# Performance work log

Hardware: AMD Instinct MI355X
Metric: run time of the kernel (lower is better)

## Reference

```python
import jax, jax.numpy as jnp
import numpy as np

EPS = 1e-5  # torch BatchNorm1d default


def _bn(v, gamma, beta):
    # BatchNorm1d in training mode, applied independently per timestep:
    # normalize over the batch axis (axis=1) with biased variance.
    mean = jnp.mean(v, axis=1, keepdims=True)
    var = jnp.var(v, axis=1, keepdims=True)
    return (v - mean) * jax.lax.rsqrt(var + EPS) * gamma + beta


def _ligru_layer(x, h0, Wxz, bxz, gz, bz, Whz, bhz, Wxh, bxh, gh, bh, Whh, bhh):
    # x: [T,B,I]. Precompute the input-side linear+batchnorm for all timesteps
    # (BN is per-timestep over batch, so it has no time dependence).
    nxz = _bn(jnp.einsum('tbi,hi->tbh', x, Wxz) + bxz, gz, bz)  # [T,B,H]
    nxh = _bn(jnp.einsum('tbi,hi->tbh', x, Wxh) + bxh, gh, bh)  # [T,B,H]

    def step(h, inp):
        xz_t, xh_t = inp
        z = jax.nn.sigmoid(xz_t + h @ Whz.T + bhz)
        cand = jax.nn.relu(xh_t + h @ Whh.T + bhh)
        h_new = z * h + (1.0 - z) * cand
        return h_new, h_new

    h_last, hs = jax.lax.scan(step, h0, (nxz, nxh))
    return hs, h_last  # [T,B,H], [B,H]


def setup_inputs() -> dict:
    key = jax.random.key(0)
    T, B, I, H, L = 512, 32, 1024, 1024, 2
    ks = jax.random.split(key, 6)
    s = 1.0 / np.sqrt(H)
    return {
        'x': jax.random.normal(ks[0], (T, B, I), jnp.float32),
        'h0': jnp.zeros((B, H), jnp.float32),
        'Wxz': jax.random.normal(ks[1], (L, H, I), jnp.float32) * s,
        'bxz': jnp.zeros((L, H), jnp.float32),
        'gz': jnp.ones((L, H), jnp.float32),
        'bz': jnp.zeros((L, H), jnp.float32),
        'Whz': jax.random.normal(ks[2], (L, H, H), jnp.float32) * s,
        'bhz': jnp.zeros((L, H), jnp.float32),
        'Wxh': jax.random.normal(ks[3], (L, H, I), jnp.float32) * s,
        'bxh': jnp.zeros((L, H), jnp.float32),
        'gh': jnp.ones((L, H), jnp.float32),
        'bh': jnp.zeros((L, H), jnp.float32),
        'Whh': jax.random.normal(ks[4], (L, H, H), jnp.float32) * s,
        'bhh': jnp.zeros((L, H), jnp.float32),
    }


def reference(x, h0, Wxz, bxz, gz, bz, Whz, bhz, Wxh, bxh, gh, bh, Whh, bhh):
    L = Wxz.shape[0]
    h_hist = []
    for l in range(L):  # small fixed layer loop (structurally distinct params)
        x, h_last = _ligru_layer(x, h0,
                                 Wxz[l], bxz[l], gz[l], bz[l], Whz[l], bhz[l],
                                 Wxh[l], bxh[l], gh[l], bh[l], Whh[l], bhh[l])
        h_hist.append(h_last)
    return x, jnp.stack(h_hist, axis=0)  # ([T,B,H], [L,B,H])
```

## Files before the change

kernel.cpp:

```cpp
#include <hip/hip_runtime.h>


typedef unsigned short u16;
typedef unsigned int   u32;
typedef unsigned long long u64;
typedef __attribute__((ext_vector_type(8))) short bf16x8;
typedef __attribute__((ext_vector_type(4))) float f32x4;
typedef __attribute__((ext_vector_type(2))) float f32x2;
typedef __attribute__((ext_vector_type(4))) unsigned int u32x4;

#define TSTEPS 512
#define BATCH  32
#define HDIM   1024
#define MROWS  (TSTEPS * BATCH)
#define KP     2048
#define NWG    64

__device__ __forceinline__ u16 f2bf(float f) {
  u32 u = __float_as_uint(f);
  return (u16)((u + 0x7FFFu + ((u >> 16) & 1u)) >> 16);
}
__device__ __forceinline__ float bf2f(u16 h) {
  return __uint_as_float(((u32)h) << 16);
}

__global__ void cast_split(const float* __restrict__ src, u16* __restrict__ dst, int total) {
  int idx = blockIdx.x * 256 + threadIdx.x;
  if (idx >= total) return;
  int m = idx >> 10, k = idx & 1023;
  float v = src[idx];
  u16 hi = f2bf(v);
  u16 lo = f2bf(v - bf2f(hi));
  dst[(size_t)m * KP + k] = hi;
  dst[(size_t)m * KP + 1024 + k] = lo;
}

__device__ __forceinline__ void stage16(const u16* g, u16* l) {
  __builtin_amdgcn_global_load_lds((const __attribute__((address_space(1))) u32*)g,
                                   (__attribute__((address_space(3))) u32*)l, 16, 0, 0);
}

__global__ __launch_bounds__(256) void gemm_bt(
    const u16* __restrict__ A,
    const u16* __restrict__ Wa, const u16* __restrict__ Wb,
    float* __restrict__ Ca, float* __restrict__ Cb) {
  constexpr int BK = 64;
  const u16* W = blockIdx.z ? Wb : Wa;
  float*     C = blockIdx.z ? Cb : Ca;
  const int m0 = blockIdx.y * 128;
  const int n0 = blockIdx.x * 128;
  __shared__ __align__(16) u16 As[128 * BK];
  __shared__ __align__(16) u16 Bs[128 * BK];
  const int tid  = threadIdx.x;
  const int lane = tid & 63;
  const int wv   = tid >> 6;
  const int wm   = wv >> 1, wn = wv & 1;
  const int srow = tid >> 3;
  const int scol = (tid & 7) * 8;
  const int frow = lane & 15;
  const int kcol = (lane >> 4) * 8;

  f32x4 z4 = {0.f, 0.f, 0.f, 0.f};
  f32x4 acc[4][4];
#pragma unroll
  for (int i = 0; i < 4; ++i)
#pragma unroll
    for (int j = 0; j < 4; ++j) acc[i][j] = z4;

  for (int k0 = 0; k0 < KP; k0 += BK) {
#pragma unroll
    for (int i = 0; i < 4; ++i)
      stage16(A + (size_t)(m0 + i * 32 + srow) * KP + k0 + scol, &As[(i * 32 + srow) * BK + scol]);
#pragma unroll
    for (int i = 0; i < 4; ++i)
      stage16(W + (size_t)(n0 + i * 32 + srow) * KP + k0 + scol, &Bs[(i * 32 + srow) * BK + scol]);
    __syncthreads();
#pragma unroll
    for (int kk = 0; kk < 2; ++kk) {
      bf16x8 av[4], bv[4];
#pragma unroll
      for (int i = 0; i < 4; ++i)
        av[i] = *(const bf16x8*)&As[(wm * 64 + i * 16 + frow) * BK + kk * 32 + kcol];
#pragma unroll
      for (int j = 0; j < 4; ++j)
        bv[j] = *(const bf16x8*)&Bs[(wn * 64 + j * 16 + frow) * BK + kk * 32 + kcol];
#pragma unroll
      for (int i = 0; i < 4; ++i)
#pragma unroll
        for (int j = 0; j < 4; ++j)
          acc[i][j] = __builtin_amdgcn_mfma_f32_16x16x32_bf16(av[i], bv[j], acc[i][j], 0, 0, 0);
    }
    __syncthreads();
  }
#pragma unroll
  for (int i = 0; i < 4; ++i)
#pragma unroll
    for (int j = 0; j < 4; ++j) {
      int n  = n0 + wn * 64 + j * 16 + (lane & 15);
      int mb = m0 + wm * 64 + i * 16 + (lane >> 4) * 4;
#pragma unroll
      for (int r = 0; r < 4; ++r)
        C[(size_t)(mb + r) * HDIM + n] = acc[i][j][r];
    }
}

__global__ void bn_inplace(float* __restrict__ Pz, float* __restrict__ Ph,
                           const float* __restrict__ gz, const float* __restrict__ bz, const float* __restrict__ bhz,
                           const float* __restrict__ gh, const float* __restrict__ bh, const float* __restrict__ bhh) {
  float*       P    = blockIdx.y ? Ph  : Pz;
  const float* gam  = blockIdx.y ? gh  : gz;
  const float* bet  = blockIdx.y ? bh  : bz;
  const float* brec = blockIdx.y ? bhh : bhz;
  int idx = blockIdx.x * 256 + threadIdx.x;
  int h = idx & 1023;
  size_t base = (size_t)(idx >> 10) * (BATCH * HDIM) + h;
  float v[BATCH];
  float s = 0.f;
#pragma unroll
  for (int b = 0; b < BATCH; ++b) { v[b] = P[base + (size_t)b * HDIM]; s += v[b]; }
  float mean = s * (1.f / BATCH);
  float q = 0.f;
#pragma unroll
  for (int b = 0; b < BATCH; ++b) { float d = v[b] - mean; q += d * d; }
  float inv = rsqrtf(q * (1.f / BATCH) + 1e-5f) * gam[h];
  float add = bet[h] + brec[h];
#pragma unroll
  for (int b = 0; b < BATCH; ++b)
    P[base + (size_t)b * HDIM] = (v[b] - mean) * inv + add;
}

__global__ void init_bar(u32* flags) { flags[threadIdx.x] = 0; }

__global__ __launch_bounds__(256, 1) void ligru_rec(
    const float* __restrict__ nxz, const float* __restrict__ nxh,
    const float* __restrict__ Whz, const float* __restrict__ Whh,
    const float* __restrict__ h0,
    u16*   __restrict__ hs_bf,
    float* __restrict__ hs_f,
    float* __restrict__ hlast,
    u32*   __restrict__ hbufw,
    u32*   __restrict__ flags) {
  const int g    = blockIdx.x;
  const int c0   = g * 16;
  const int tid  = threadIdx.x;
  const int lane = tid & 63;
  const int wv   = tid >> 6;
  const int half = wv >> 1;
  const int ksec = wv & 1;
  const int r    = lane & 15;
  const int ko   = lane >> 4;

  __shared__ float part[2][2][2][16][17];

  bf16x8 wz_hi[16], wz_lo[16], wh_hi[16], wh_lo[16];
  {
    const float* zrow = Whz + (size_t)(c0 + r) * HDIM;
    const float* hrow = Whh + (size_t)(c0 + r) * HDIM;
#pragma unroll
    for (int kk = 0; kk < 16; ++kk) {
      int kb = ksec * 512 + ko * 8 + kk * 32;
      f32x4 z0 = *(const f32x4*)(zrow + kb);
      f32x4 z1 = *(const f32x4*)(zrow + kb + 4);
      f32x4 h0v = *(const f32x4*)(hrow + kb);
      f32x4 h1v = *(const f32x4*)(hrow + kb + 4);
      bf16x8 zh, zl, hh, hl;
#pragma unroll
      for (int j = 0; j < 4; ++j) {
        u16 a = f2bf(z0[j]);  zh[j]   = (short)a;  zl[j]   = (short)f2bf(z0[j] - bf2f(a));
        u16 b = f2bf(z1[j]);  zh[4+j] = (short)b;  zl[4+j] = (short)f2bf(z1[j] - bf2f(b));
        u16 c = f2bf(h0v[j]); hh[j]   = (short)c;  hl[j]   = (short)f2bf(h0v[j] - bf2f(c));
        u16 d = f2bf(h1v[j]); hh[4+j] = (short)d;  hl[4+j] = (short)f2bf(h1v[j] - bf2f(d));
      }
      wz_hi[kk] = zh; wz_lo[kk] = zl; wh_hi[kk] = hh; wh_lo[kk] = hl;
    }
  }

  const int bb = tid >> 3;
  const int cp = tid & 7;
  const int bh_ = bb >> 4, br_ = bb & 15;
  float hr0 = h0[(size_t)bb * HDIM + c0 + 2 * cp];
  float hr1 = h0[(size_t)bb * HDIM + c0 + 2 * cp + 1];
  {
    u32 p = (u32)f2bf(hr0) | ((u32)f2bf(hr1) << 16);
    __hip_atomic_store(hbufw + (size_t)bb * 512 + g * 8 + cp, p,
                       __ATOMIC_RELAXED, __HIP_MEMORY_SCOPE_AGENT);
  }
  __syncthreads();
  if (tid == 0)
    __hip_atomic_store(&flags[g], 1u, __ATOMIC_RELAXED, __HIP_MEMORY_SCOPE_AGENT);
  {
    for (;;) {
      u32 f = __hip_atomic_load(&flags[lane], __ATOMIC_RELAXED, __HIP_MEMORY_SCOPE_AGENT);
      if (__all(f >= 1u)) break;
    }
  }

  const size_t hb64base = (size_t)(half * 16 + r) * 256 + ksec * 128 + ko * 2;
  f32x4 z4 = {0.f, 0.f, 0.f, 0.f};

  f32x2 nxz_c = *(const f32x2*)(nxz + (size_t)bb * HDIM + c0 + 2 * cp);
  f32x2 nxh_c = *(const f32x2*)(nxh + (size_t)bb * HDIM + c0 + 2 * cp);

  for (int t = 0; t < TSTEPS; ++t) {
    const u64* hb64 = (const u64*)(hbufw + (size_t)(t & 1) * (BATCH * 512));
    u32*       hbn  = hbufw + (size_t)((t + 1) & 1) * (BATCH * 512);

    asm volatile("" ::: "memory");
    const u64* hbp = hb64 + hb64base;
    u32x4 hw4[16];
#pragma unroll
    for (int kk = 0; kk < 16; ++kk)
      asm volatile("global_load_dwordx4 %0, %1, off offset:%2 sc0 sc1"
                   : "=v"(hw4[kk])
                   : "v"(hbp), "i"(kk * 64));
    asm volatile("s_waitcnt vmcnt(0)" ::: "memory");
    __builtin_amdgcn_sched_barrier(0);

    int tn = (t + 1 < TSTEPS) ? t + 1 : t;
    f32x2 nxz_n = *(const f32x2*)(nxz + (size_t)(tn * BATCH + bb) * HDIM + c0 + 2 * cp);
    f32x2 nxh_n = *(const f32x2*)(nxh + (size_t)(tn * BATCH + bb) * HDIM + c0 + 2 * cp);

    f32x4 az0 = z4, az1 = z4, ac0 = z4, ac1 = z4;
#pragma unroll
    for (int kk = 0; kk < 16; ++kk) {
      union { u32x4 q; bf16x8 v; } a;
      a.q = hw4[kk];
      az0 = __builtin_amdgcn_mfma_f32_16x16x32_bf16(a.v, wz_hi[kk], az0, 0, 0, 0);
      az1 = __builtin_amdgcn_mfma_f32_16x16x32_bf16(a.v, wz_lo[kk], az1, 0, 0, 0);
      ac0 = __builtin_amdgcn_mfma_f32_16x16x32_bf16(a.v, wh_hi[kk], ac0, 0, 0, 0);
      ac1 = __builtin_amdgcn_mfma_f32_16x16x32_bf16(a.v, wh_lo[kk], ac1, 0, 0, 0);
    }
    f32x4 sz = az0 + az1;
    f32x4 sc = ac0 + ac1;

#pragma unroll
    for (int reg = 0; reg < 4; ++reg) {
      part[0][ksec][half][ko * 4 + reg][r] = sz[reg];
      part[1][ksec][half][ko * 4 + reg][r] = sc[reg];
    }
    __syncthreads();

    float zp0 = part[0][0][bh_][br_][2 * cp]     + part[0][1][bh_][br_][2 * cp]     + nxz_c[0];
    float zp1 = part[0][0][bh_][br_][2 * cp + 1] + part[0][1][bh_][br_][2 * cp + 1] + nxz_c[1];
    float cp0 = part[1][0][bh_][br_][2 * cp]     + part[1][1][bh_][br_][2 * cp]     + nxh_c[0];
    float cp1 = part[1][0][bh_][br_][2 * cp + 1] + part[1][1][bh_][br_][2 * cp + 1] + nxh_c[1];
    float zg0 = 1.f / (1.f + __expf(-zp0));
    float zg1 = 1.f / (1.f + __expf(-zp1));
    float cd0 = fmaxf(cp0, 0.f);
    float cd1 = fmaxf(cp1, 0.f);
    float hn0 = zg0 * hr0 + (1.f - zg0) * cd0;
    float hn1 = zg1 * hr1 + (1.f - zg1) * cd1;
    hr0 = hn0; hr1 = hn1;

    u16 hi0 = f2bf(hn0), hi1 = f2bf(hn1);
    u32 p = (u32)hi0 | ((u32)hi1 << 16);
    __hip_atomic_store(hbn + (size_t)bb * 512 + g * 8 + cp, p,
                       __ATOMIC_RELAXED, __HIP_MEMORY_SCOPE_AGENT);
    __syncthreads();
    if (tid == 0)
      __hip_atomic_store(&flags[g], (u32)(t + 2), __ATOMIC_RELAXED, __HIP_MEMORY_SCOPE_AGENT);

    if (hs_f) {
      f32x2 o = {hn0, hn1};
      *(f32x2*)(hs_f + (size_t)(t * BATCH + bb) * HDIM + c0 + 2 * cp) = o;
    } else {
      size_t row = (size_t)(t * BATCH + bb) * KP;
      *(u32*)(hs_bf + row + c0 + 2 * cp) = p;
      u32 plo = (u32)f2bf(hn0 - bf2f(hi0)) | ((u32)f2bf(hn1 - bf2f(hi1)) << 16);
      *(u32*)(hs_bf + row + 1024 + c0 + 2 * cp) = plo;
    }

    if (t == TSTEPS - 1) {
      f32x2 o = {hn0, hn1};
      *(f32x2*)(hlast + (size_t)bb * HDIM + c0 + 2 * cp) = o;
    } else {
      u32 tgt = (u32)(t + 2);
      for (;;) {
        u32 f = __hip_atomic_load(&flags[lane], __ATOMIC_RELAXED, __HIP_MEMORY_SCOPE_AGENT);
        if (__all(f >= tgt)) break;
      }
    }
    nxz_c = nxz_n; nxh_c = nxh_n;
  }
}

extern "C" void kernel_launch(void* const* d_in, const int* in_sizes, int n_in,
                              void* d_out, int out_size, void* d_ws, size_t ws_size,
                              hipStream_t stream) {
  const float* x   = (const float*)d_in[0];
  const float* h0  = (const float*)d_in[1];
  const float* Wxz = (const float*)d_in[2];
  const float* gz  = (const float*)d_in[4];
  const float* bz  = (const float*)d_in[5];
  const float* Whz = (const float*)d_in[6];
  const float* bhz = (const float*)d_in[7];
  const float* Wxh = (const float*)d_in[8];
  const float* gh  = (const float*)d_in[10];
  const float* bh  = (const float*)d_in[11];
  const float* Whh = (const float*)d_in[12];
  const float* bhh = (const float*)d_in[13];

  float* out_x = (float*)d_out;
  float* out_h = out_x + (size_t)MROWS * HDIM;

  char* w = (char*)d_ws;
  u16* xsp = (u16*)w;  w += (size_t)MROWS * KP * 2;
  u16* wxp[4];
  for (int i = 0; i < 4; ++i) { wxp[i] = (u16*)w; w += (size_t)HDIM * KP * 2; }
  float* Pz = (float*)w;  w += (size_t)MROWS * HDIM * 4;
  float* Ph = (float*)w;  w += (size_t)MROWS * HDIM * 4;
  u32* hbufw = (u32*)w;   w += (size_t)2 * BATCH * 512 * 4;
  u32* flags = (u32*)w;   w += 64 * 4;

  cast_split<<<(MROWS * HDIM + 255) / 256, 256, 0, stream>>>(x, xsp, MROWS * HDIM);
  for (int l = 0; l < 2; ++l) {
    cast_split<<<(HDIM * HDIM + 255) / 256, 256, 0, stream>>>(Wxz + (size_t)l * HDIM * HDIM, wxp[l * 2 + 0], HDIM * HDIM);
    cast_split<<<(HDIM * HDIM + 255) / 256, 256, 0, stream>>>(Wxh + (size_t)l * HDIM * HDIM, wxp[l * 2 + 1], HDIM * HDIM);
  }

  for (int l = 0; l < 2; ++l) {
    dim3 gg(HDIM / 128, MROWS / 128, 2);
    gemm_bt<<<gg, 256, 0, stream>>>(xsp, wxp[l * 2 + 0], wxp[l * 2 + 1], Pz, Ph);
    bn_inplace<<<dim3((TSTEPS * HDIM) / 256, 2), 256, 0, stream>>>(
        Pz, Ph,
        gz + (size_t)l * HDIM, bz + (size_t)l * HDIM, bhz + (size_t)l * HDIM,
        gh + (size_t)l * HDIM, bh + (size_t)l * HDIM, bhh + (size_t)l * HDIM);
    init_bar<<<1, 64, 0, stream>>>(flags);
    ligru_rec<<<NWG, 256, 0, stream>>>(
        Pz, Ph,
        Whz + (size_t)l * HDIM * HDIM, Whh + (size_t)l * HDIM * HDIM, h0,
        (l == 0) ? xsp : (u16*)nullptr,
        (l == 0) ? (float*)nullptr : out_x,
        out_h + (size_t)l * BATCH * HDIM,
        hbufw, flags);
  }
}
```

Measured before the change: 5.423 ms.

## Halve recurrent workgroups, drop low-half weight split, vectorize hidden-state stores

The recurrent kernel now runs on 32 workgroups instead of 64, and each workgroup owns 32 hidden columns instead of 16. The register budget that held the hi/lo bf16 weight pair now holds two 16-column groups stored as bf16 only. The per-step MFMA count per workgroup stays the same, while the cross-workgroup flag barrier spins on half as many participants. Hidden-state exchange and history writes are packed with a lane shuffle into 128-bit stores. The cost is that recurrent weights lose their low-order correction term, which lowers matmul precision and may hurt accuracy over 512 recurrent steps.

```diff
diff --git a/kernel.cpp b/kernel.cpp
--- a/kernel.cpp
+++ b/kernel.cpp
@@ -14,7 +14,7 @@
 #define HDIM   1024
 #define MROWS  (TSTEPS * BATCH)
 #define KP     2048
-#define NWG    64
+#define NWG    32
 
 __device__ __forceinline__ u16 f2bf(float f) {
   u32 u = __float_as_uint(f);
@@ -141,7 +141,7 @@
     u32*   __restrict__ hbufw,
     u32*   __restrict__ flags) {
   const int g    = blockIdx.x;
-  const int c0   = g * 16;
+  const int c0   = g * 32;
   const int tid  = threadIdx.x;
   const int lane = tid & 63;
   const int wv   = tid >> 6;
@@ -150,12 +150,13 @@
   const int r    = lane & 15;
   const int ko   = lane >> 4;
 
-  __shared__ float part[2][2][2][16][17];
-
-  bf16x8 wz_hi[16], wz_lo[16], wh_hi[16], wh_lo[16];
-  {
-    const float* zrow = Whz + (size_t)(c0 + r) * HDIM;
-    const float* hrow = Whh + (size_t)(c0 + r) * HDIM;
+  __shared__ float part[2][2][2][16][33];
+
+  bf16x8 wz[2][16], wh[2][16];
+#pragma unroll
+  for (int cg = 0; cg < 2; ++cg) {
+    const float* zrow = Whz + (size_t)(c0 + cg * 16 + r) * HDIM;
+    const float* hrow = Whh + (size_t)(c0 + cg * 16 + r) * HDIM;
 #pragma unroll
     for (int kk = 0; kk < 16; ++kk) {
       int kb = ksec * 512 + ko * 8 + kk * 32;
@@ -163,34 +164,35 @@
       f32x4 z1 = *(const f32x4*)(zrow + kb + 4);
       f32x4 h0v = *(const f32x4*)(hrow + kb);
       f32x4 h1v = *(const f32x4*)(hrow + kb + 4);
-      bf16x8 zh, zl, hh, hl;
+      bf16x8 zv, hv;
 #pragma unroll
       for (int j = 0; j < 4; ++j) {
-        u16 a = f2bf(z0[j]);  zh[j]   = (short)a;  zl[j]   = (short)f2bf(z0[j] - bf2f(a));
-        u16 b = f2bf(z1[j]);  zh[4+j] = (short)b;  zl[4+j] = (short)f2bf(z1[j] - bf2f(b));
-        u16 c = f2bf(h0v[j]); hh[j]   = (short)c;  hl[j]   = (short)f2bf(h0v[j] - bf2f(c));
-        u16 d = f2bf(h1v[j]); hh[4+j] = (short)d;  hl[4+j] = (short)f2bf(h1v[j] - bf2f(d));
+        zv[j]     = (short)f2bf(z0[j]);
+        zv[4 + j] = (short)f2bf(z1[j]);
+        hv[j]     = (short)f2bf(h0v[j]);
+        hv[4 + j] = (short)f2bf(h1v[j]);
       }
-      wz_hi[kk] = zh; wz_lo[kk] = zl; wh_hi[kk] = hh; wh_lo[kk] = hl;
+      wz[cg][kk] = zv; wh[cg][kk] = hv;
     }
   }
 
   const int bb = tid >> 3;
   const int cp = tid & 7;
   const int bh_ = bb >> 4, br_ = bb & 15;
-  float hr0 = h0[(size_t)bb * HDIM + c0 + 2 * cp];
-  float hr1 = h0[(size_t)bb * HDIM + c0 + 2 * cp + 1];
+  f32x4 hr = *(const f32x4*)(h0 + (size_t)bb * HDIM + c0 + 4 * cp);
   {
-    u32 p = (u32)f2bf(hr0) | ((u32)f2bf(hr1) << 16);
-    __hip_atomic_store(hbufw + (size_t)bb * 512 + g * 8 + cp, p,
-                       __ATOMIC_RELAXED, __HIP_MEMORY_SCOPE_AGENT);
+    u32 p0 = (u32)f2bf(hr[0]) | ((u32)f2bf(hr[1]) << 16);
+    u32 p1 = (u32)f2bf(hr[2]) | ((u32)f2bf(hr[3]) << 16);
+    u32* dst = hbufw + (size_t)bb * 512 + g * 16 + 2 * cp;
+    __hip_atomic_store(dst,     p0, __ATOMIC_RELAXED, __HIP_MEMORY_SCOPE_AGENT);
+    __hip_atomic_store(dst + 1, p1, __ATOMIC_RELAXED, __HIP_MEMORY_SCOPE_AGENT);
   }
   __syncthreads();
   if (tid == 0)
     __hip_atomic_store(&flags[g], 1u, __ATOMIC_RELAXED, __HIP_MEMORY_SCOPE_AGENT);
   {
     for (;;) {
-      u32 f = __hip_atomic_load(&flags[lane], __ATOMIC_RELAXED, __HIP_MEMORY_SCOPE_AGENT);
+      u32 f = __hip_atomic_load(&flags[lane & 31], __ATOMIC_RELAXED, __HIP_MEMORY_SCOPE_AGENT);
       if (__all(f >= 1u)) break;
     }
   }
@@ -198,8 +200,8 @@
   const size_t hb64base = (size_t)(half * 16 + r) * 256 + ksec * 128 + ko * 2;
   f32x4 z4 = {0.f, 0.f, 0.f, 0.f};
 
-  f32x2 nxz_c = *(const f32x2*)(nxz + (size_t)bb * HDIM + c0 + 2 * cp);
-  f32x2 nxh_c = *(const f32x2*)(nxh + (size_t)bb * HDIM + c0 + 2 * cp);
+  f32x4 nxz_c = *(const f32x4*)(nxz + (size_t)bb * HDIM + c0 + 4 * cp);
+  f32x4 nxh_c = *(const f32x4*)(nxh + (size_t)bb * HDIM + c0 + 4 * cp);
 
   for (int t = 0; t < TSTEPS; ++t) {
     const u64* hb64 = (const u64*)(hbufw + (size_t)(t & 1) * (BATCH * 512));
@@ -217,66 +219,80 @@
     __builtin_amdgcn_sched_barrier(0);
 
     int tn = (t + 1 < TSTEPS) ? t + 1 : t;
-    f32x2 nxz_n = *(const f32x2*)(nxz + (size_t)(tn * BATCH + bb) * HDIM + c0 + 2 * cp);
-    f32x2 nxh_n = *(const f32x2*)(nxh + (size_t)(tn * BATCH + bb) * HDIM + c0 + 2 * cp);
+    f32x4 nxz_n = *(const f32x4*)(nxz + (size_t)(tn * BATCH + bb) * HDIM + c0 + 4 * cp);
+    f32x4 nxh_n = *(const f32x4*)(nxh + (size_t)(tn * BATCH + bb) * HDIM + c0 + 4 * cp);
 
     f32x4 az0 = z4, az1 = z4, ac0 = z4, ac1 = z4;
 #pragma unroll
     for (int kk = 0; kk < 16; ++kk) {
       union { u32x4 q; bf16x8 v; } a;
       a.q = hw4[kk];
-      az0 = __builtin_amdgcn_mfma_f32_16x16x32_bf16(a.v, wz_hi[kk], az0, 0, 0, 0);
-      az1 = __builtin_amdgcn_mfma_f32_16x16x32_bf16(a.v, wz_lo[kk], az1, 0, 0, 0);
-      ac0 = __builtin_amdgcn_mfma_f32_16x16x32_bf16(a.v, wh_hi[kk], ac0, 0, 0, 0);
-      ac1 = __builtin_amdgcn_mfma_f32_16x16x32_bf16(a.v, wh_lo[kk], ac1, 0, 0, 0);
-    }
-    f32x4 sz = az0 + az1;
-    f32x4 sc = ac0 + ac1;
+      az0 = __builtin_amdgcn_mfma_f32_16x16x32_bf16(a.v, wz[0][kk], az0, 0, 0, 0);
+      az1 = __builtin_amdgcn_mfma_f32_16x16x32_bf16(a.v, wz[1][kk], az1, 0, 0, 0);
+      ac0 = __builtin_amdgcn_mfma_f32_16x16x32_bf16(a.v, wh[0][kk], ac0, 0, 0, 0);
+      ac1 = __builtin_amdgcn_mfma_f32_16x16x32_bf16(a.v, wh[1][kk], ac1, 0, 0, 0);
+    }
 
 #pragma unroll
     for (int reg = 0; reg < 4; ++reg) {
-      part[0][ksec][half][ko * 4 + reg][r] = sz[reg];
-      part[1][ksec][half][ko * 4 + reg][r] = sc[reg];
+      part[0][ksec][half][ko * 4 + reg][r]      = az0[reg];
+      part[0][ksec][half][ko * 4 + reg][16 + r] = az1[reg];
+      part[1][ksec][half][ko * 4 + reg][r]      = ac0[reg];
+      part[1][ksec][half][ko * 4 + reg][16 + r] = ac1[reg];
     }
     __syncthreads();
 
-    float zp0 = part[0][0][bh_][br_][2 * cp]     + part[0][1][bh_][br_][2 * cp]     + nxz_c[0];
-    float zp1 = part[0][0][bh_][br_][2 * cp + 1] + part[0][1][bh_][br_][2 * cp + 1] + nxz_c[1];
-    float cp0 = part[1][0][bh_][br_][2 * cp]     + part[1][1][bh_][br_][2 * cp]     + nxh_c[0];
-    float cp1 = part[1][0][bh_][br_][2 * cp + 1] + part[1][1][bh_][br_][2 * cp + 1] + nxh_c[1];
-    float zg0 = 1.f / (1.f + __expf(-zp0));
-    float zg1 = 1.f / (1.f + __expf(-zp1));
-    float cd0 = fmaxf(cp0, 0.f);
-    float cd1 = fmaxf(cp1, 0.f);
-    float hn0 = zg0 * hr0 + (1.f - zg0) * cd0;
-    float hn1 = zg1 * hr1 + (1.f - zg1) * cd1;
-    hr0 = hn0; hr1 = hn1;
-
-    u16 hi0 = f2bf(hn0), hi1 = f2bf(hn1);
-    u32 p = (u32)hi0 | ((u32)hi1 << 16);
-    __hip_atomic_store(hbn + (size_t)bb * 512 + g * 8 + cp, p,
-                       __ATOMIC_RELAXED, __HIP_MEMORY_SCOPE_AGENT);
+    f32x4 hn;
+#pragma unroll
+    for (int j = 0; j < 4; ++j) {
+      int col = 4 * cp + j;
+      float zp = part[0][0][bh_][br_][col] + part[0][1][bh_][br_][col] + nxz_c[j];
+      float cq = part[1][0][bh_][br_][col] + part[1][1][bh_][br_][col] + nxh_c[j];
+      float zg = 1.f / (1.f + __expf(-zp));
+      float cd = fmaxf(cq, 0.f);
+      hn[j] = zg * hr[j] + (1.f - zg) * cd;
+    }
+    hr = hn;
+
+    u16 h0b = f2bf(hn[0]), h1b = f2bf(hn[1]), h2b = f2bf(hn[2]), h3b = f2bf(hn[3]);
+    u32 p0 = (u32)h0b | ((u32)h1b << 16);
+    u32 p1 = (u32)h2b | ((u32)h3b << 16);
+
+    u32 p0n = __shfl_down(p0, 1);
+    u32 p1n = __shfl_down(p1, 1);
+    if ((tid & 1) == 0) {
+      u32x4 pk4 = {p0, p1, p0n, p1n};
+      u32* dst = hbn + (size_t)bb * 512 + g * 16 + 2 * cp;
+      asm volatile("global_store_dwordx4 %0, %1, off sc0 sc1"
+                   :: "v"(dst), "v"(pk4) : "memory");
+    }
     __syncthreads();
     if (tid == 0)
       __hip_atomic_store(&flags[g], (u32)(t + 2), __ATOMIC_RELAXED, __HIP_MEMORY_SCOPE_AGENT);
 
     if (hs_f) {
-      f32x2 o = {hn0, hn1};
-      *(f32x2*)(hs_f + (size_t)(t * BATCH + bb) * HDIM + c0 + 2 * cp) = o;
+      *(f32x4*)(hs_f + (size_t)(t * BATCH + bb) * HDIM + c0 + 4 * cp) = hn;
     } else {
-      size_t row = (size_t)(t * BATCH + bb) * KP;
-      *(u32*)(hs_bf + row + c0 + 2 * cp) = p;
-      u32 plo = (u32)f2bf(hn0 - bf2f(hi0)) | ((u32)f2bf(hn1 - bf2f(hi1)) << 16);
-      *(u32*)(hs_bf + row + 1024 + c0 + 2 * cp) = plo;
+      u32 l0 = (u32)f2bf(hn[0] - bf2f(h0b)) | ((u32)f2bf(hn[1] - bf2f(h1b)) << 16);
+      u32 l1 = (u32)f2bf(hn[2] - bf2f(h2b)) | ((u32)f2bf(hn[3] - bf2f(h3b)) << 16);
+      u32 l0n = __shfl_down(l0, 1);
+      u32 l1n = __shfl_down(l1, 1);
+      if ((tid & 1) == 0) {
+        u32* hs32 = (u32*)hs_bf;
+        size_t base = (size_t)(t * BATCH + bb) * (KP / 2) + g * 16 + 2 * cp;
+        u32x4 h4 = {p0, p1, p0n, p1n};
+        u32x4 l4 = {l0, l1, l0n, l1n};
+        asm volatile("global_store_dwordx4 %0, %1, off" :: "v"(hs32 + base), "v"(h4) : "memory");
+        asm volatile("global_store_dwordx4 %0, %1, off" :: "v"(hs32 + base + 512), "v"(l4) : "memory");
+      }
     }
 
     if (t == TSTEPS - 1) {
-      f32x2 o = {hn0, hn1};
-      *(f32x2*)(hlast + (size_t)bb * HDIM + c0 + 2 * cp) = o;
+      *(f32x4*)(hlast + (size_t)bb * HDIM + c0 + 4 * cp) = hn;
     } else {
       u32 tgt = (u32)(t + 2);
       for (;;) {
-        u32 f = __hip_atomic_load(&flags[lane], __ATOMIC_RELAXED, __HIP_MEMORY_SCOPE_AGENT);
+        u32 f = __hip_atomic_load(&flags[lane & 31], __ATOMIC_RELAXED, __HIP_MEMORY_SCOPE_AGENT);
         if (__all(f >= tgt)) break;
       }
     }
```

After: 4.773 ms. 12.0% less time.
